# Performance work log

Measured on AMD Instinct MI355X. Metric: run time of the kernel, lower is better.

Reference implementation:

```python
import jax, jax.numpy as jnp
import numpy as np

B, N, C = 2, 6, 80
FH, FW = 16, 44
D = 112
NX = NY = 128
NZ = 1
OGH, OGW = 256, 704
D_BOUND = (2.0, 58.0, 0.5)
VOXEL_SIZE = np.array([0.8, 0.8, 8.0], dtype=np.float32)
VOXEL_COORD = np.array([-51.2 + 0.4, -51.2 + 0.4, -5.0 + 4.0], dtype=np.float32)
VOXEL_NUM = np.array([NX, NY, NZ], dtype=np.int32)


def setup_inputs() -> dict:
    key = jax.random.key(0)
    k1, k2 = jax.random.split(key)
    context = jax.random.normal(k1, (B * N, C, FH, FW), jnp.float32)
    depth_logits = jax.random.normal(k2, (B * N, D, FH, FW), jnp.float32)
    # realistic camera matrices (random matrices would not be invertible / physical)
    intrin = np.tile(np.eye(4, dtype=np.float32), (B, N, 1, 1))
    intrin[..., 0, 0] = 560.0
    intrin[..., 1, 1] = 560.0
    intrin[..., 0, 2] = OGW / 2.0
    intrin[..., 1, 2] = OGH / 2.0
    ida = np.tile(np.eye(4, dtype=np.float32), (B, N, 1, 1))
    s2e = np.tile(np.eye(4, dtype=np.float32), (B, N, 1, 1))
    # cam axes (x right, y down, z forward) -> ego axes (x fwd, y left, z up)
    M = np.array([[0., 0., 1.], [-1., 0., 0.], [0., -1., 0.]], dtype=np.float32)
    for n in range(N):
        yaw = 2.0 * np.pi * n / N
        cy, sy = np.cos(yaw), np.sin(yaw)
        R = np.array([[cy, -sy, 0.], [sy, cy, 0.], [0., 0., 1.]], dtype=np.float32)
        s2e[:, n, :3, :3] = R @ M
        s2e[:, n, :3, 3] = np.array([1.5 * cy, 1.5 * sy, 1.6], dtype=np.float32)
    bda = np.tile(np.eye(4, dtype=np.float32), (B, 1, 1))
    return dict(context=context, depth_logits=depth_logits,
                sensor2ego_mat=jnp.asarray(s2e), intrin_mat=jnp.asarray(intrin),
                ida_mat=jnp.asarray(ida), bda_mat=jnp.asarray(bda))


def _frustum():
    # [D, FH, FW, 4] pixel-plane frustum: (u, v, depth, 1)
    d = jnp.arange(D_BOUND[0], D_BOUND[1], D_BOUND[2], dtype=jnp.float32) + D_BOUND[2] / 2.0
    d = jnp.broadcast_to(d[:, None, None], (D, FH, FW))
    xs = jnp.broadcast_to(jnp.linspace(0.0, OGW - 1.0, FW)[None, None, :], (D, FH, FW))
    ys = jnp.broadcast_to(jnp.linspace(0.0, OGH - 1.0, FH)[None, :, None], (D, FH, FW))
    return jnp.stack([xs, ys, d, jnp.ones_like(d)], -1)


def reference(context, depth_logits, sensor2ego_mat, intrin_mat, ida_mat, bda_mat):
    # ---- get_geometry ----
    pts = _frustum()[None, None, ..., None]                       # [1,1,D,FH,FW,4,1]
    ida_inv = jnp.linalg.inv(ida_mat).reshape(B, N, 1, 1, 1, 4, 4)
    pts = ida_inv @ pts
    pts = jnp.concatenate([pts[..., :2, :] * pts[..., 2:3, :], pts[..., 2:, :]], axis=-2)
    combine = (sensor2ego_mat @ jnp.linalg.inv(intrin_mat)).reshape(B, N, 1, 1, 1, 4, 4)
    pts = combine @ pts
    bda = bda_mat.reshape(B, 1, 1, 1, 1, 4, 4)
    geom = (bda @ pts)[..., :3, 0]                                # [B,N,D,FH,FW,3] ego coords

    # ---- voxel indices ----
    vsize = jnp.asarray(VOXEL_SIZE)
    vcoord = jnp.asarray(VOXEL_COORD)
    vnum = jnp.asarray(VOXEL_NUM)
    idx = jnp.floor((geom - (vcoord - vsize / 2.0)) / vsize).astype(jnp.int32)
    valid = jnp.all((idx >= 0) & (idx < vnum), axis=-1)           # [B,N,D,FH,FW]

    # ---- lift: depth-weighted outer product ----
    depth = jax.nn.softmax(depth_logits, axis=1).reshape(B, N, D, FH, FW)
    ctx = context.reshape(B, N, C, FH, FW)
    feat = jnp.einsum('bndhw,bnchw->bndhwc', depth, ctx)          # [B,N,D,FH,FW,C]
    feat = feat * valid[..., None]

    # ---- splat: scatter-add into BEV grid ----
    b_idx = jnp.arange(B, dtype=jnp.int32)[:, None, None, None, None]
    lin = b_idx * (NY * NX) + idx[..., 1] * NX + idx[..., 0]
    lin = jnp.where(valid, lin, 0)                                # invalid feats already zeroed
    bev = jax.ops.segment_sum(feat.reshape(-1, C), lin.reshape(-1),
                              num_segments=B * NY * NX)
    return bev.reshape(B, NY, NX, C).transpose(0, 3, 1, 2)        # [B,C,NY,NX]
```

## Files before the change

kernel.cpp:

```cpp
#include <hip/hip_runtime.h>
#include <hip/hip_bf16.h>
#include <math.h>

#define B_ 2
#define N_ 6
#define C_ 80
#define FH_ 16
#define FW_ 44
#define D_ 112
#define NX_ 128
#define NY_ 128
#define NCOL (B_ * N_ * FH_ * FW_)
#define NCELL (B_ * NY_ * NX_)
#define MAXT (NCOL * D_)
#define GB_CELLS 16

typedef __hip_bfloat16 bf16;
typedef unsigned short u16;

__device__ __forceinline__ float loadf(const void* p, int i, int isbf) {
  if (isbf) return __bfloat162float(((const bf16*)p)[i]);
  return ((const float*)p)[i];
}

__device__ __forceinline__ int probe_tbf(const void* logits) {
  int lane = threadIdx.x & 63;
  unsigned short v = ((const unsigned short*)logits)[2 * lane];
  int e = (v >> 7) & 0xFF;
  int ok = (v == 0) || (e >= 110 && e <= 136);
  return __popcll(__ballot(ok)) > 42;
}
__device__ __forceinline__ int probe_mbf(const void* intrin) {
  float v = ((const float*)intrin)[0];
  return !(v > 100.f && v < 1.0e6f);
}

__device__ __forceinline__ void inv4(const float m[16], float invOut[16]) {
  float inv[16];
  inv[0]  =  m[5]*m[10]*m[15] - m[5]*m[11]*m[14] - m[9]*m[6]*m[15] + m[9]*m[7]*m[14] + m[13]*m[6]*m[11] - m[13]*m[7]*m[10];
  inv[4]  = -m[4]*m[10]*m[15] + m[4]*m[11]*m[14] + m[8]*m[6]*m[15] - m[8]*m[7]*m[14] - m[12]*m[6]*m[11] + m[12]*m[7]*m[10];
  inv[8]  =  m[4]*m[9]*m[15]  - m[4]*m[11]*m[13] - m[8]*m[5]*m[15] + m[8]*m[7]*m[13] + m[12]*m[5]*m[11] - m[12]*m[7]*m[9];
  inv[12] = -m[4]*m[9]*m[14]  + m[4]*m[10]*m[13] + m[8]*m[5]*m[14] - m[8]*m[6]*m[13] - m[12]*m[5]*m[10] + m[12]*m[6]*m[9];
  inv[1]  = -m[1]*m[10]*m[15] + m[1]*m[11]*m[14] + m[9]*m[2]*m[15] - m[9]*m[3]*m[14] - m[13]*m[2]*m[11] + m[13]*m[3]*m[10];
  inv[5]  =  m[0]*m[10]*m[15] - m[0]*m[11]*m[14] - m[8]*m[2]*m[15] + m[8]*m[3]*m[14] + m[12]*m[2]*m[11] - m[12]*m[3]*m[10];
  inv[9]  = -m[0]*m[9]*m[15]  + m[0]*m[11]*m[13] + m[8]*m[1]*m[15] - m[8]*m[3]*m[13] - m[12]*m[1]*m[11] + m[12]*m[3]*m[9];
  inv[13] =  m[0]*m[9]*m[14]  - m[0]*m[10]*m[13] - m[8]*m[1]*m[14] + m[8]*m[2]*m[13] + m[12]*m[1]*m[10] - m[12]*m[2]*m[9];
  inv[2]  =  m[1]*m[6]*m[15]  - m[1]*m[7]*m[14]  - m[5]*m[2]*m[15] + m[5]*m[3]*m[14] + m[13]*m[2]*m[7]  - m[13]*m[3]*m[6];
  inv[6]  = -m[0]*m[6]*m[15]  + m[0]*m[7]*m[14]  + m[4]*m[2]*m[15] - m[4]*m[3]*m[14] - m[12]*m[2]*m[7]  + m[12]*m[3]*m[6];
  inv[10] =  m[0]*m[5]*m[15]  - m[0]*m[7]*m[13]  - m[4]*m[1]*m[15] + m[4]*m[3]*m[13] + m[12]*m[1]*m[7]  - m[12]*m[3]*m[5];
  inv[14] = -m[0]*m[5]*m[14]  + m[0]*m[6]*m[13]  + m[4]*m[1]*m[14] - m[4]*m[2]*m[13] - m[12]*m[1]*m[6]  + m[12]*m[2]*m[5];
  inv[3]  = -m[1]*m[6]*m[11]  + m[1]*m[7]*m[10]  + m[5]*m[2]*m[11] - m[5]*m[3]*m[10] - m[9]*m[2]*m[7]   + m[9]*m[3]*m[6];
  inv[7]  =  m[0]*m[6]*m[11]  - m[0]*m[7]*m[10]  - m[4]*m[2]*m[11] + m[4]*m[3]*m[10] + m[8]*m[2]*m[7]   - m[8]*m[3]*m[6];
  inv[11] = -m[0]*m[5]*m[11]  + m[0]*m[7]*m[9]   + m[4]*m[1]*m[11] - m[4]*m[3]*m[9]  - m[8]*m[1]*m[7]   + m[8]*m[3]*m[5];
  inv[15] =  m[0]*m[5]*m[10]  - m[0]*m[6]*m[9]   - m[4]*m[1]*m[10] + m[4]*m[2]*m[9]  + m[8]*m[1]*m[6]   - m[8]*m[2]*m[5];
  float det = m[0]*inv[0] + m[1]*inv[4] + m[2]*inv[8] + m[3]*inv[12];
  det = 1.0f / det;
  for (int i = 0; i < 16; i++) invOut[i] = inv[i] * det;
}

__device__ __forceinline__ void mul4(const float A[16], const float Bm[16], float Cm[16]) {
  for (int i = 0; i < 4; i++)
    for (int j = 0; j < 4; j++) {
      float s = 0.f;
      for (int k = 0; k < 4; k++) s += A[i * 4 + k] * Bm[k * 4 + j];
      Cm[i * 4 + j] = s;
    }
}

__device__ __forceinline__ void fold_mats(const void* s2e, const void* intrin,
                                          const void* ida, const void* bda, int bn,
                                          float Ainv[16], float M[16]) {
  const int mbf = probe_mbf(intrin);
  const int b = bn / N_;
  float S[16], I[16], A[16], Bd[16], Iinv[16], Cm[16];
  for (int i = 0; i < 16; i++) {
    S[i]  = loadf(s2e,    bn * 16 + i, mbf);
    I[i]  = loadf(intrin, bn * 16 + i, mbf);
    A[i]  = loadf(ida,    bn * 16 + i, mbf);
    Bd[i] = loadf(bda,    b * 16 + i, mbf);
  }
  inv4(I, Iinv);
  inv4(A, Ainv);
  mul4(S, Iinv, Cm);
  mul4(Bd, Cm, M);
}

__device__ __forceinline__ int geom_cell(const float Ai[16], const float M[16],
                                         int bn, int h, int w, int d) {
  float u = (float)w * (703.0f / 43.0f);
  float v = (float)h * 17.0f;
  float dep = 2.25f + 0.5f * (float)d;
  float p0 = ((Ai[0] * u + Ai[1] * v) + Ai[2] * dep) + Ai[3];
  float p1 = ((Ai[4] * u + Ai[5] * v) + Ai[6] * dep) + Ai[7];
  float p2 = ((Ai[8] * u + Ai[9] * v) + Ai[10] * dep) + Ai[11];
  float p3 = ((Ai[12] * u + Ai[13] * v) + Ai[14] * dep) + Ai[15];
  float q0 = p0 * p2, q1 = p1 * p2;
  float gx = ((M[0] * q0 + M[1] * q1) + M[2] * p2) + M[3] * p3;
  float gy = ((M[4] * q0 + M[5] * q1) + M[6] * p2) + M[7] * p3;
  float gz = ((M[8] * q0 + M[9] * q1) + M[10] * p2) + M[11] * p3;
  int ix = (int)floorf((gx + 51.2f) / 0.8f);
  int iy = (int)floorf((gy + 51.2f) / 0.8f);
  int iz = (int)floorf((gz + 5.0f) / 8.0f);
  bool valid = (ix >= 0) && (ix < NX_) && (iy >= 0) && (iy < NY_) && (iz == 0);
  int b = bn / N_;
  return valid ? (b * (NY_ * NX_) + iy * NX_ + ix) : -1;
}

__global__ __launch_bounds__(64) void lss_stage1(
    const void* __restrict__ ctx, const void* __restrict__ logits,
    const void* __restrict__ s2e, const void* __restrict__ intrin,
    const void* __restrict__ ida, const void* __restrict__ bda,
    float* __restrict__ ctx_t, float* __restrict__ logits_t,
    int* __restrict__ counts) {
  const int tid = threadIdx.x;
  const int col = blockIdx.x;
  const int tbf = probe_tbf(logits);
  const int gtid = col * 64 + tid;
  const int NT = NCOL * 64;

  for (int i = gtid; i < NCOL * C_; i += NT) {
    int c2 = i / C_, c = i - c2 * C_;
    int bn2 = c2 / (FH_ * FW_), r = c2 - bn2 * (FH_ * FW_);
    int h2 = r / FW_, w2 = r - h2 * FW_;
    ctx_t[i] = loadf(ctx, ((bn2 * C_ + c) * FH_ + h2) * FW_ + w2, tbf);
  }
  for (int i = gtid; i < NCOL * D_; i += NT) {
    int c2 = i / D_, d = i - c2 * D_;
    int bn2 = c2 / (FH_ * FW_), r = c2 - bn2 * (FH_ * FW_);
    int h2 = r / FW_, w2 = r - h2 * FW_;
    logits_t[i] = loadf(logits, ((bn2 * D_ + d) * FH_ + h2) * FW_ + w2, tbf);
  }

  const int w = col % FW_;
  const int h = (col / FW_) % FH_;
  const int bn = col / (FW_ * FH_);
  float Ai[16], M[16];
  fold_mats(s2e, intrin, ida, bda, bn, Ai, M);
  __shared__ int s_cell[D_];
  s_cell[tid] = geom_cell(Ai, M, bn, h, w, tid);
  if (tid < D_ - 64) s_cell[tid + 64] = geom_cell(Ai, M, bn, h, w, tid + 64);
  __syncthreads();
  for (int d = tid; d < D_; d += 64) {
    int vcell = s_cell[d];
    if (vcell >= 0 && (d == 0 || s_cell[d - 1] != vcell)) atomicAdd(&counts[vcell], 1);
  }
}

__global__ __launch_bounds__(1024) void lss_scan(const int* __restrict__ counts,
                                                 int* __restrict__ offsets,
                                                 int* __restrict__ cursors) {
  __shared__ int s[1024];
  const int t = threadIdx.x;
  const int base = t * 32;
  int local[32];
  int sum = 0;
  for (int j = 0; j < 32; j++) { local[j] = counts[base + j]; sum += local[j]; }
  s[t] = sum;
  __syncthreads();
  for (int st = 1; st < 1024; st <<= 1) {
    int v = (t >= st) ? s[t - st] : 0;
    __syncthreads();
    s[t] += v;
    __syncthreads();
  }
  int run = s[t] - sum;
  for (int j = 0; j < 32; j++) {
    offsets[base + j] = run;
    cursors[base + j] = run;
    run += local[j];
  }
}

__global__ __launch_bounds__(64) void lss_fill(
    const float* __restrict__ logits_t,
    const void* __restrict__ s2e, const void* __restrict__ intrin,
    const void* __restrict__ ida, const void* __restrict__ bda,
    int* __restrict__ cursors, u16* __restrict__ colids, float* __restrict__ wts) {
  const int tid = threadIdx.x;
  const int col = blockIdx.x;
  const int w = col % FW_;
  const int h = (col / FW_) % FH_;
  const int bn = col / (FW_ * FH_);
  float Ai[16], M[16];
  fold_mats(s2e, intrin, ida, bda, bn, Ai, M);

  __shared__ float s_w[D_];
  __shared__ int s_cell[D_];

  float l0 = logits_t[col * D_ + tid];
  float l1 = (tid < D_ - 64) ? logits_t[col * D_ + 64 + tid] : -1e30f;
  float m = fmaxf(l0, l1);
  for (int s = 32; s > 0; s >>= 1) m = fmaxf(m, __shfl_xor(m, s));
  float e0 = expf(l0 - m);
  float e1 = (tid < D_ - 64) ? expf(l1 - m) : 0.f;
  float sum = e0 + e1;
  for (int s = 32; s > 0; s >>= 1) sum += __shfl_xor(sum, s);
  float inv_sum = 1.0f / sum;

  s_w[tid] = e0;
  s_cell[tid] = geom_cell(Ai, M, bn, h, w, tid);
  if (tid < D_ - 64) {
    s_w[tid + 64] = e1;
    s_cell[tid + 64] = geom_cell(Ai, M, bn, h, w, tid + 64);
  }
  __syncthreads();

  for (int d = tid; d < D_; d += 64) {
    int vcell = s_cell[d];
    if (vcell >= 0 && (d == 0 || s_cell[d - 1] != vcell)) {
      float acc = s_w[d];
      for (int j = d + 1; j < D_ && s_cell[j] == vcell; ++j) acc += s_w[j];
      int pos = atomicAdd(&cursors[vcell], 1);
      colids[pos] = (u16)col;
      wts[pos] = acc * inv_sum;
    }
  }
}

__global__ __launch_bounds__(1024) void lss_gather(
    const float* __restrict__ ctx_t, const int* __restrict__ counts,
    const int* __restrict__ offsets, const u16* __restrict__ colids,
    const float* __restrict__ wts, const void* __restrict__ logits,
    void* __restrict__ out) {
  __shared__ float s_out[GB_CELLS * 84];
  const int tbf = probe_tbf(logits);
  const int tid = threadIdx.x;
  const int wv = tid >> 6;
  const int ln = tid & 63;
  const int sl = ln >> 2;
  const int g = ln & 3;
  const int cell = blockIdx.x * GB_CELLS + wv;
  const int n = counts[cell];
  const int off = offsets[cell];

  float acc[20];
#pragma unroll
  for (int i = 0; i < 20; i++) acc[i] = 0.f;

  for (int j = sl; j < n; j += 16) {
    int colj = colids[off + j];
    float wj = wts[off + j];
    const float4* cp = (const float4*)(ctx_t + colj * C_ + g * 20);
#pragma unroll
    for (int q = 0; q < 5; q++) {
      float4 v = cp[q];
      acc[q * 4 + 0] += wj * v.x;
      acc[q * 4 + 1] += wj * v.y;
      acc[q * 4 + 2] += wj * v.z;
      acc[q * 4 + 3] += wj * v.w;
    }
  }
#pragma unroll
  for (int msk = 4; msk <= 32; msk <<= 1) {
#pragma unroll
    for (int i = 0; i < 20; i++) acc[i] += __shfl_xor(acc[i], msk);
  }
  if (sl == 0) {
#pragma unroll
    for (int i = 0; i < 20; i++) s_out[wv * 84 + g * 20 + i] = acc[i];
  }
  __syncthreads();

  const int x = tid & 15;
  const int c0 = tid >> 4;
  const int cell0 = blockIdx.x * GB_CELLS;
  const int b = cell0 >> 14;
  const int yx0 = cell0 & 16383;
  if (tbf) {
    bf16* o = (bf16*)out;
    o[(size_t)(b * C_ + c0) * (NY_ * NX_) + yx0 + x] = __float2bfloat16(s_out[x * 84 + c0]);
    if (c0 < 16)
      o[(size_t)(b * C_ + 64 + c0) * (NY_ * NX_) + yx0 + x] = __float2bfloat16(s_out[x * 84 + 64 + c0]);
  } else {
    float* o = (float*)out;
    o[(size_t)(b * C_ + c0) * (NY_ * NX_) + yx0 + x] = s_out[x * 84 + c0];
    if (c0 < 16)
      o[(size_t)(b * C_ + 64 + c0) * (NY_ * NX_) + yx0 + x] = s_out[x * 84 + 64 + c0];
  }
}

extern "C" void kernel_launch(void* const* d_in, const int* in_sizes, int n_in,
                              void* d_out, int out_size, void* d_ws, size_t ws_size,
                              hipStream_t stream) {
  const void* ctx = d_in[0];
  const void* logits = d_in[1];
  const void* s2e = d_in[2];
  const void* intrin = d_in[3];
  const void* ida = d_in[4];
  const void* bda = d_in[5];

  float* wsf = (float*)d_ws;
  int* counts     = (int*)(wsf + 512);
  int* offsets    = (int*)(wsf + 512 + NCELL);
  int* cursors    = (int*)(wsf + 512 + 2 * NCELL);
  float* ctx_t    = wsf + 512 + 3 * NCELL;
  float* logits_t = ctx_t + NCOL * C_;
  u16* colids     = (u16*)(logits_t + NCOL * D_);
  float* wts      = (float*)((float*)colids + MAXT / 2);

  hipMemsetAsync(counts, 0, NCELL * sizeof(int), stream);
  lss_stage1<<<NCOL, 64, 0, stream>>>(ctx, logits, s2e, intrin, ida, bda,
                                      ctx_t, logits_t, counts);
  lss_scan<<<1, 1024, 0, stream>>>(counts, offsets, cursors);
  lss_fill<<<NCOL, 64, 0, stream>>>(logits_t, s2e, intrin, ida, bda,
                                    cursors, colids, wts);
  lss_gather<<<NCELL / GB_CELLS, 1024, 0, stream>>>(ctx_t, counts, offsets, colids, wts,
                                                    logits, d_out);
}
```

Baseline: 218.0 us.

## Fuse four LSS stages into one cooperative persistent kernel with grid syncs

Replaces the four separate launches (transpose+count, scan, fill, gather) with one cooperative kernel of 256 blocks of 1024 threads that separates the phases with grid.sync. The transposes now go through a shared-memory tile so both reads and writes are coalesced, the scan becomes a two-level block-parallel scan, and each wave handles a frustum column or a group of cells. The aim is to remove launch gaps and the serial single-block scan. The cost is grid-wide barrier overhead and fewer threads per item in the gather phase.

```diff
diff --git a/kernel.cpp b/kernel.cpp
--- a/kernel.cpp
+++ b/kernel.cpp
@@ -1,19 +1,25 @@
 #include <hip/hip_runtime.h>
 #include <hip/hip_bf16.h>
+#include <hip/hip_cooperative_groups.h>
 #include <math.h>
+
+namespace cg = cooperative_groups;
 
 #define B_ 2
 #define N_ 6
 #define C_ 80
 #define FH_ 16
 #define FW_ 44
+#define HW_ (FH_ * FW_)
 #define D_ 112
 #define NX_ 128
 #define NY_ 128
-#define NCOL (B_ * N_ * FH_ * FW_)
+#define NCOL (B_ * N_ * HW_)
 #define NCELL (B_ * NY_ * NX_)
 #define MAXT (NCOL * D_)
-#define GB_CELLS 16
+#define NBLK 256
+#define NTHR 1024
+#define NWAVES (NBLK * (NTHR / 64))
 
 typedef __hip_bfloat16 bf16;
 typedef unsigned short u16;
@@ -106,176 +112,200 @@
   return valid ? (b * (NY_ * NX_) + iy * NX_ + ix) : -1;
 }
 
-__global__ __launch_bounds__(64) void lss_stage1(
+__global__ __launch_bounds__(NTHR, 4) void lss_mega(
     const void* __restrict__ ctx, const void* __restrict__ logits,
     const void* __restrict__ s2e, const void* __restrict__ intrin,
     const void* __restrict__ ida, const void* __restrict__ bda,
     float* __restrict__ ctx_t, float* __restrict__ logits_t,
-    int* __restrict__ counts) {
+    int* __restrict__ counts, int* __restrict__ offsets,
+    int* __restrict__ cursors, int* __restrict__ gsums,
+    u16* __restrict__ colids, float* __restrict__ wts,
+    void* __restrict__ out) {
+  cg::grid_group grid = cg::this_grid();
+  __shared__ union {
+    float tile[16][65];
+    struct { int cell[16][D_]; float w[16][D_]; } cf;
+    int tmp[256];
+    float stage[64 * 81];
+  } sm;
   const int tid = threadIdx.x;
-  const int col = blockIdx.x;
+  const int bid = blockIdx.x;
+  const int lane = tid & 63;
+  const int widx = tid >> 6;
+  const int wgid = bid * (NTHR / 64) + widx;
   const int tbf = probe_tbf(logits);
-  const int gtid = col * 64 + tid;
-  const int NT = NCOL * 64;
-
-  for (int i = gtid; i < NCOL * C_; i += NT) {
-    int c2 = i / C_, c = i - c2 * C_;
-    int bn2 = c2 / (FH_ * FW_), r = c2 - bn2 * (FH_ * FW_);
-    int h2 = r / FW_, w2 = r - h2 * FW_;
-    ctx_t[i] = loadf(ctx, ((bn2 * C_ + c) * FH_ + h2) * FW_ + w2, tbf);
-  }
-  for (int i = gtid; i < NCOL * D_; i += NT) {
-    int c2 = i / D_, d = i - c2 * D_;
-    int bn2 = c2 / (FH_ * FW_), r = c2 - bn2 * (FH_ * FW_);
-    int h2 = r / FW_, w2 = r - h2 * FW_;
-    logits_t[i] = loadf(logits, ((bn2 * D_ + d) * FH_ + h2) * FW_ + w2, tbf);
-  }
-
-  const int w = col % FW_;
-  const int h = (col / FW_) % FH_;
-  const int bn = col / (FW_ * FH_);
-  float Ai[16], M[16];
-  fold_mats(s2e, intrin, ida, bda, bn, Ai, M);
-  __shared__ int s_cell[D_];
-  s_cell[tid] = geom_cell(Ai, M, bn, h, w, tid);
-  if (tid < D_ - 64) s_cell[tid + 64] = geom_cell(Ai, M, bn, h, w, tid + 64);
-  __syncthreads();
-  for (int d = tid; d < D_; d += 64) {
-    int vcell = s_cell[d];
-    if (vcell >= 0 && (d == 0 || s_cell[d - 1] != vcell)) atomicAdd(&counts[vcell], 1);
-  }
-}
-
-__global__ __launch_bounds__(1024) void lss_scan(const int* __restrict__ counts,
-                                                 int* __restrict__ offsets,
-                                                 int* __restrict__ cursors) {
-  __shared__ int s[1024];
-  const int t = threadIdx.x;
-  const int base = t * 32;
-  int local[32];
-  int sum = 0;
-  for (int j = 0; j < 32; j++) { local[j] = counts[base + j]; sum += local[j]; }
-  s[t] = sum;
-  __syncthreads();
-  for (int st = 1; st < 1024; st <<= 1) {
-    int v = (t >= st) ? s[t - st] : 0;
-    __syncthreads();
-    s[t] += v;
-    __syncthreads();
-  }
-  int run = s[t] - sum;
-  for (int j = 0; j < 32; j++) {
-    offsets[base + j] = run;
-    cursors[base + j] = run;
-    run += local[j];
-  }
-}
-
-__global__ __launch_bounds__(64) void lss_fill(
-    const float* __restrict__ logits_t,
-    const void* __restrict__ s2e, const void* __restrict__ intrin,
-    const void* __restrict__ ida, const void* __restrict__ bda,
-    int* __restrict__ cursors, u16* __restrict__ colids, float* __restrict__ wts) {
-  const int tid = threadIdx.x;
-  const int col = blockIdx.x;
-  const int w = col % FW_;
-  const int h = (col / FW_) % FH_;
-  const int bn = col / (FW_ * FH_);
-  float Ai[16], M[16];
-  fold_mats(s2e, intrin, ida, bda, bn, Ai, M);
-
-  __shared__ float s_w[D_];
-  __shared__ int s_cell[D_];
-
-  float l0 = logits_t[col * D_ + tid];
-  float l1 = (tid < D_ - 64) ? logits_t[col * D_ + 64 + tid] : -1e30f;
-  float m = fmaxf(l0, l1);
-  for (int s = 32; s > 0; s >>= 1) m = fmaxf(m, __shfl_xor(m, s));
-  float e0 = expf(l0 - m);
-  float e1 = (tid < D_ - 64) ? expf(l1 - m) : 0.f;
-  float sum = e0 + e1;
-  for (int s = 32; s > 0; s >>= 1) sum += __shfl_xor(sum, s);
-  float inv_sum = 1.0f / sum;
-
-  s_w[tid] = e0;
-  s_cell[tid] = geom_cell(Ai, M, bn, h, w, tid);
-  if (tid < D_ - 64) {
-    s_w[tid + 64] = e1;
-    s_cell[tid + 64] = geom_cell(Ai, M, bn, h, w, tid + 64);
-  }
-  __syncthreads();
-
-  for (int d = tid; d < D_; d += 64) {
-    int vcell = s_cell[d];
-    if (vcell >= 0 && (d == 0 || s_cell[d - 1] != vcell)) {
-      float acc = s_w[d];
-      for (int j = d + 1; j < D_ && s_cell[j] == vcell; ++j) acc += s_w[j];
-      int pos = atomicAdd(&cursors[vcell], 1);
-      colids[pos] = (u16)col;
-      wts[pos] = acc * inv_sum;
-    }
-  }
-}
-
-__global__ __launch_bounds__(1024) void lss_gather(
-    const float* __restrict__ ctx_t, const int* __restrict__ counts,
-    const int* __restrict__ offsets, const u16* __restrict__ colids,
-    const float* __restrict__ wts, const void* __restrict__ logits,
-    void* __restrict__ out) {
-  __shared__ float s_out[GB_CELLS * 84];
-  const int tbf = probe_tbf(logits);
-  const int tid = threadIdx.x;
-  const int wv = tid >> 6;
-  const int ln = tid & 63;
-  const int sl = ln >> 2;
-  const int g = ln & 3;
-  const int cell = blockIdx.x * GB_CELLS + wv;
-  const int n = counts[cell];
-  const int off = offsets[cell];
-
-  float acc[20];
-#pragma unroll
-  for (int i = 0; i < 20; i++) acc[i] = 0.f;
-
-  for (int j = sl; j < n; j += 16) {
-    int colj = colids[off + j];
-    float wj = wts[off + j];
-    const float4* cp = (const float4*)(ctx_t + colj * C_ + g * 20);
-#pragma unroll
-    for (int q = 0; q < 5; q++) {
-      float4 v = cp[q];
-      acc[q * 4 + 0] += wj * v.x;
-      acc[q * 4 + 1] += wj * v.y;
-      acc[q * 4 + 2] += wj * v.z;
-      acc[q * 4 + 3] += wj * v.w;
-    }
-  }
-#pragma unroll
-  for (int msk = 4; msk <= 32; msk <<= 1) {
-#pragma unroll
-    for (int i = 0; i < 20; i++) acc[i] += __shfl_xor(acc[i], msk);
-  }
-  if (sl == 0) {
-#pragma unroll
-    for (int i = 0; i < 20; i++) s_out[wv * 84 + g * 20 + i] = acc[i];
-  }
-  __syncthreads();
-
-  const int x = tid & 15;
-  const int c0 = tid >> 4;
-  const int cell0 = blockIdx.x * GB_CELLS;
-  const int b = cell0 >> 14;
-  const int yx0 = cell0 & 16383;
-  if (tbf) {
-    bf16* o = (bf16*)out;
-    o[(size_t)(b * C_ + c0) * (NY_ * NX_) + yx0 + x] = __float2bfloat16(s_out[x * 84 + c0]);
-    if (c0 < 16)
-      o[(size_t)(b * C_ + 64 + c0) * (NY_ * NX_) + yx0 + x] = __float2bfloat16(s_out[x * 84 + 64 + c0]);
-  } else {
-    float* o = (float*)out;
-    o[(size_t)(b * C_ + c0) * (NY_ * NX_) + yx0 + x] = s_out[x * 84 + c0];
-    if (c0 < 16)
-      o[(size_t)(b * C_ + 64 + c0) * (NY_ * NX_) + yx0 + x] = s_out[x * 84 + 64 + c0];
+
+  const int CT = B_ * N_ * (C_ / 16) * (HW_ / 64);
+  const int LT = B_ * N_ * (D_ / 16) * (HW_ / 64);
+  {
+    const int ty = tid >> 6, tx = tid & 63;
+    const int tx2 = tid & 15, ty2 = tid >> 4;
+    for (int t = bid; t < CT + LT; t += NBLK) {
+      if (t < CT) {
+        int bn = t / 55, rem = t % 55;
+        int c0 = (rem / 11) * 16, hw0 = (rem % 11) * 64;
+        sm.tile[ty][tx] = loadf(ctx, (bn * C_ + c0 + ty) * HW_ + hw0 + tx, tbf);
+        __syncthreads();
+        ctx_t[(bn * HW_ + hw0 + ty2) * C_ + c0 + tx2] = sm.tile[tx2][ty2];
+      } else {
+        int t2 = t - CT;
+        int bn = t2 / 77, rem = t2 % 77;
+        int d0 = (rem / 11) * 16, hw0 = (rem % 11) * 64;
+        sm.tile[ty][tx] = loadf(logits, (bn * D_ + d0 + ty) * HW_ + hw0 + tx, tbf);
+        __syncthreads();
+        logits_t[(bn * HW_ + hw0 + ty2) * D_ + d0 + tx2] = sm.tile[tx2][ty2];
+      }
+      __syncthreads();
+    }
+  }
+
+  for (int i = 0; i < 3; i++) {
+    int col = wgid + i * NWAVES;
+    int active = col < NCOL;
+    if (active) {
+      int w = col % FW_, h = (col / FW_) % FH_, bn = col / HW_;
+      float Ai[16], M[16];
+      fold_mats(s2e, intrin, ida, bda, bn, Ai, M);
+      sm.cf.cell[widx][lane] = geom_cell(Ai, M, bn, h, w, lane);
+      if (lane < D_ - 64)
+        sm.cf.cell[widx][lane + 64] = geom_cell(Ai, M, bn, h, w, lane + 64);
+    }
+    __syncthreads();
+    if (active) {
+      for (int d = lane; d < D_; d += 64) {
+        int vc = sm.cf.cell[widx][d];
+        if (vc >= 0 && (d == 0 || sm.cf.cell[widx][d - 1] != vc))
+          atomicAdd(&counts[vc], 1);
+      }
+    }
+    __syncthreads();
+  }
+  grid.sync();
+
+  int myExcl = 0;
+  {
+    int myVal = 0;
+    if (tid < 128) { myVal = counts[bid * 128 + tid]; sm.tmp[tid] = myVal; }
+    __syncthreads();
+    for (int st = 1; st < 128; st <<= 1) {
+      int v = 0;
+      if (tid < 128 && tid >= st) v = sm.tmp[tid - st];
+      __syncthreads();
+      if (tid < 128) sm.tmp[tid] += v;
+      __syncthreads();
+    }
+    if (tid < 128) myExcl = sm.tmp[tid] - myVal;
+    if (tid == 127) gsums[bid] = sm.tmp[127];
+  }
+  grid.sync();
+  {
+    if (tid < 256) sm.tmp[tid] = (tid < bid) ? gsums[tid] : 0;
+    __syncthreads();
+    for (int st = 128; st > 0; st >>= 1) {
+      if (tid < st) sm.tmp[tid] += sm.tmp[tid + st];
+      __syncthreads();
+    }
+    int gpref = sm.tmp[0];
+    if (tid < 128) {
+      int v = gpref + myExcl;
+      offsets[bid * 128 + tid] = v;
+      cursors[bid * 128 + tid] = v;
+    }
+    __syncthreads();
+  }
+  grid.sync();
+
+  for (int i = 0; i < 3; i++) {
+    int col = wgid + i * NWAVES;
+    int active = col < NCOL;
+    float inv_sum = 0.f;
+    if (active) {
+      int w = col % FW_, h = (col / FW_) % FH_, bn = col / HW_;
+      float Ai[16], M[16];
+      fold_mats(s2e, intrin, ida, bda, bn, Ai, M);
+      float l0 = logits_t[col * D_ + lane];
+      float l1 = (lane < D_ - 64) ? logits_t[col * D_ + 64 + lane] : -1e30f;
+      float m = fmaxf(l0, l1);
+      for (int s = 32; s > 0; s >>= 1) m = fmaxf(m, __shfl_xor(m, s));
+      float e0 = expf(l0 - m);
+      float e1 = (lane < D_ - 64) ? expf(l1 - m) : 0.f;
+      float sum = e0 + e1;
+      for (int s = 32; s > 0; s >>= 1) sum += __shfl_xor(sum, s);
+      inv_sum = 1.0f / sum;
+      sm.cf.cell[widx][lane] = geom_cell(Ai, M, bn, h, w, lane);
+      sm.cf.w[widx][lane] = e0;
+      if (lane < D_ - 64) {
+        sm.cf.cell[widx][lane + 64] = geom_cell(Ai, M, bn, h, w, lane + 64);
+        sm.cf.w[widx][lane + 64] = e1;
+      }
+    }
+    __syncthreads();
+    if (active) {
+      for (int d = lane; d < D_; d += 64) {
+        int vc = sm.cf.cell[widx][d];
+        if (vc >= 0 && (d == 0 || sm.cf.cell[widx][d - 1] != vc)) {
+          float acc = sm.cf.w[widx][d];
+          for (int j = d + 1; j < D_ && sm.cf.cell[widx][j] == vc; ++j)
+            acc += sm.cf.w[widx][j];
+          int pos = atomicAdd(&cursors[vc], 1);
+          colids[pos] = (u16)col;
+          wts[pos] = acc * inv_sum;
+        }
+      }
+    }
+    __syncthreads();
+  }
+  grid.sync();
+
+  for (int p = 0; p < 2; p++) {
+    int cb = bid + p * NBLK;
+    int cell0 = cb * 64;
+    int cl = widx * 4 + (lane >> 4);
+    int sl = (lane >> 2) & 3;
+    int g = lane & 3;
+    int cell = cell0 + cl;
+    int n = counts[cell];
+    int off = offsets[cell];
+    float acc[20];
+#pragma unroll
+    for (int i = 0; i < 20; i++) acc[i] = 0.f;
+    for (int j = sl; j < n; j += 4) {
+      int colj = colids[off + j];
+      float wj = wts[off + j];
+      const float4* cp = (const float4*)(ctx_t + colj * C_ + g * 20);
+#pragma unroll
+      for (int q = 0; q < 5; q++) {
+        float4 v = cp[q];
+        acc[q * 4 + 0] += wj * v.x;
+        acc[q * 4 + 1] += wj * v.y;
+        acc[q * 4 + 2] += wj * v.z;
+        acc[q * 4 + 3] += wj * v.w;
+      }
+    }
+#pragma unroll
+    for (int msk = 4; msk <= 8; msk <<= 1) {
+#pragma unroll
+      for (int i = 0; i < 20; i++) acc[i] += __shfl_xor(acc[i], msk);
+    }
+    if (sl == 0) {
+#pragma unroll
+      for (int i = 0; i < 20; i++) sm.stage[cl * 81 + g * 20 + i] = acc[i];
+    }
+    __syncthreads();
+    {
+      int b = cell0 >> 14;
+      int yx0 = cell0 & 16383;
+      int x = tid & 63;
+#pragma unroll
+      for (int it = 0; it < 5; it++) {
+        int c = (tid >> 6) + it * 16;
+        float val = sm.stage[x * 81 + c];
+        size_t oi = ((size_t)(b * C_ + c) << 14) + yx0 + x;
+        if (tbf) ((bf16*)out)[oi] = __float2bfloat16(val);
+        else ((float*)out)[oi] = val;
+      }
+    }
+    __syncthreads();
   }
 }
 
@@ -289,21 +319,20 @@
   const void* ida = d_in[4];
   const void* bda = d_in[5];
 
-  float* wsf = (float*)d_ws;
-  int* counts     = (int*)(wsf + 512);
-  int* offsets    = (int*)(wsf + 512 + NCELL);
-  int* cursors    = (int*)(wsf + 512 + 2 * NCELL);
-  float* ctx_t    = wsf + 512 + 3 * NCELL;
+  int* counts     = (int*)d_ws;
+  int* offsets    = counts + NCELL;
+  int* cursors    = offsets + NCELL;
+  int* gsums      = cursors + NCELL;
+  float* ctx_t    = (float*)(gsums + 256);
   float* logits_t = ctx_t + NCOL * C_;
   u16* colids     = (u16*)(logits_t + NCOL * D_);
-  float* wts      = (float*)((float*)colids + MAXT / 2);
+  float* wts      = (float*)(colids + MAXT);
+  void* outp      = d_out;
 
   hipMemsetAsync(counts, 0, NCELL * sizeof(int), stream);
-  lss_stage1<<<NCOL, 64, 0, stream>>>(ctx, logits, s2e, intrin, ida, bda,
-                                      ctx_t, logits_t, counts);
-  lss_scan<<<1, 1024, 0, stream>>>(counts, offsets, cursors);
-  lss_fill<<<NCOL, 64, 0, stream>>>(logits_t, s2e, intrin, ida, bda,
-                                    cursors, colids, wts);
-  lss_gather<<<NCELL / GB_CELLS, 1024, 0, stream>>>(ctx_t, counts, offsets, colids, wts,
-                                                    logits, d_out);
-}
+  void* args[] = {(void*)&ctx, (void*)&logits, (void*)&s2e, (void*)&intrin,
+                  (void*)&ida, (void*)&bda, (void*)&ctx_t, (void*)&logits_t,
+                  (void*)&counts, (void*)&offsets, (void*)&cursors, (void*)&gsums,
+                  (void*)&colids, (void*)&wts, (void*)&outp};
+  hipLaunchCooperativeKernel((void*)lss_mega, dim3(NBLK), dim3(NTHR), args, 0, stream);
+}
```

Measured after the change: 467.9 us. 115% more time.
